# Performance work log

Hardware: AMD Instinct MI355X
Metric: run time of the kernel (lower is better)

Reference implementation:

```python
import jax, jax.numpy as jnp
import numpy as np

B, S, D = 2, 2048, 2048
H, KV = 16, 4
HD = D // H          # 128
QPK = H // KV        # queries per kv head


def setup_inputs() -> dict:
    key = jax.random.key(0)
    ks = jax.random.split(key, 8)
    x = jax.random.normal(ks[0], (B, S, D), jnp.float32)
    mask = jnp.zeros((1, 1, S, S), jnp.float32)  # unused (causal flash path)
    # RoPE tables: theta=10000, shape (S, HD//2)
    inv_freq = 1.0 / (10000.0 ** (jnp.arange(0, HD, 2, dtype=jnp.float32) / HD))
    freqs = jnp.outer(jnp.arange(S, dtype=jnp.float32), inv_freq)
    freqs_cos, freqs_sin = jnp.cos(freqs), jnp.sin(freqs)
    sc = 0.02
    Wq = jax.random.normal(ks[1], (D, H * HD), jnp.float32) * sc
    bq = jnp.zeros((H * HD,), jnp.float32)
    Wk = jax.random.normal(ks[2], (D, KV * HD), jnp.float32) * sc
    bk = jnp.zeros((KV * HD,), jnp.float32)
    Wv = jax.random.normal(ks[3], (D, KV * HD), jnp.float32) * sc
    bv = jnp.zeros((KV * HD,), jnp.float32)
    Wo = jax.random.normal(ks[4], (D, D), jnp.float32) * sc  # bias=False
    return dict(x=x, mask=mask, freqs_cos=freqs_cos, freqs_sin=freqs_sin,
                Wq=Wq, bq=bq, Wk=Wk, bk=bk, Wv=Wv, bv=bv, Wo=Wo)


def _rope(t, cos, sin):
    # t: [B, S, nH, HD]; interleaved-pair rotation as in apply_rope
    tr = t.reshape(t.shape[:-1] + (-1, 2))
    r, i = tr[..., 0], tr[..., 1]
    c = cos[None, :, None, :]
    s = sin[None, :, None, :]
    out = jnp.stack([r * c - i * s, r * s + i * c], axis=-1)
    return out.reshape(t.shape)


def reference(x, mask, freqs_cos, freqs_sin, Wq, bq, Wk, bk, Wv, bv, Wo):
    b, s, d = x.shape
    q = (x @ Wq + bq).reshape(b, s, H, HD)
    k = (x @ Wk + bk).reshape(b, s, KV, HD)
    v = (x @ Wv + bv).reshape(b, s, KV, HD)
    cos, sin = freqs_cos[:s], freqs_sin[:s]
    q = _rope(q, cos, sin)
    k = _rope(k, cos, sin)
    # GQA: repeat_interleave kv heads to match query heads
    k = jnp.repeat(k, QPK, axis=2)
    v = jnp.repeat(v, QPK, axis=2)
    q = q.transpose(0, 2, 1, 3)  # [B, H, S, HD]
    k = k.transpose(0, 2, 1, 3)
    v = v.transpose(0, 2, 1, 3)
    scores = jnp.einsum('bhqd,bhkd->bhqk', q, k) / jnp.sqrt(jnp.float32(HD))
    causal = jnp.tril(jnp.ones((s, s), bool))
    scores = jnp.where(causal[None, None], scores, jnp.finfo(scores.dtype).min)
    attn = jax.nn.softmax(scores, axis=-1)
    out = jnp.einsum('bhqk,bhkd->bhqd', attn, v)
    out = out.transpose(0, 2, 1, 3).reshape(b, s, d)
    return out @ Wo
```

## Files before the change

kernel.cpp:

```cpp
#include <hip/hip_runtime.h>


#define B_  2
#define S_  2048
#define D_  2048
#define H_  16
#define KV_ 4
#define HD_ 128
#define NQKV 3072

typedef unsigned short ushort_t;
typedef __attribute__((ext_vector_type(8))) __bf16 bf16x8;
typedef __attribute__((ext_vector_type(4))) float  f32x4;

__device__ __forceinline__ ushort_t f2bf(float f) {
    unsigned u = __float_as_uint(f);
    u += 0x7FFFu + ((u >> 16) & 1u);
    return (ushort_t)(u >> 16);
}
__device__ __forceinline__ float bf2f(ushort_t h) {
    return __uint_as_float(((unsigned)h) << 16);
}

__device__ __forceinline__ void g2l16(const void* g, void* l) {
    __builtin_amdgcn_global_load_lds(
        (const __attribute__((address_space(1))) unsigned int*)g,
        (__attribute__((address_space(3))) unsigned int*)l, 16, 0, 0);
}


__global__ __launch_bounds__(256) void k_cvt_x(const float* __restrict__ x,
                                               ushort_t* __restrict__ xb, int n4) {
    int i = blockIdx.x * 256 + threadIdx.x;
    if (i < n4) {
        float4 v = ((const float4*)x)[i];
        ushort4 o;
        o.x = f2bf(v.x); o.y = f2bf(v.y); o.z = f2bf(v.z); o.w = f2bf(v.w);
        ((ushort4*)xb)[i] = o;
    }
}

__global__ __launch_bounds__(256) void k_transpose(const float* __restrict__ src,
                                                   ushort_t* __restrict__ dst,
                                                   int R, int C) {
    __shared__ float tile[32][33];
    int c0 = blockIdx.x * 32, r0 = blockIdx.y * 32;
    int tx = threadIdx.x, ty = threadIdx.y;
    for (int i = ty; i < 32; i += 8)
        tile[i][tx] = src[(size_t)(r0 + i) * C + c0 + tx];
    __syncthreads();
    for (int i = ty; i < 32; i += 8)
        dst[(size_t)(c0 + i) * R + r0 + tx] = f2bf(tile[tx][i]);
}

__global__ __launch_bounds__(256) void k_bias(const float* bq, const float* bk,
                                              const float* bv, float* bb) {
    int i = blockIdx.x * 256 + threadIdx.x;
    if (i < 3072)
        bb[i] = (i < 2048) ? bq[i] : (i < 2560) ? bk[i - 2048] : bv[i - 2560];
}


__global__ __launch_bounds__(256, 3) void k_gemm(const ushort_t* __restrict__ A,
                                                 const ushort_t* __restrict__ Bt,
                                                 void* __restrict__ Cp,
                                                 const float* __restrict__ bias,
                                                 int M, int N, int K, int out_bf16) {
    __shared__ __align__(16) ushort_t As[128 * 32];
    __shared__ __align__(16) ushort_t Bs[128 * 32];
    int t = threadIdx.x;
    int w = t >> 6, lane = t & 63, quad = lane >> 4, l16 = lane & 15;
    int m0 = blockIdx.y * 128, n0 = blockIdx.x * 128;
    int wm = (w >> 1) * 64, wn = (w & 1) * 64;
    f32x4 acc[4][4] = {};

    int ldrow = t >> 2, ldcol = (t & 3) * 8;
    const ushort_t* Ag = A + (size_t)(m0 + ldrow) * K + ldcol;
    const ushort_t* Bg = Bt + (size_t)(n0 + ldrow) * K + ldcol;
    char* AsW = (char*)As + (t >> 6) * 1024;
    char* BsW = (char*)Bs + (t >> 6) * 1024;

    for (int k0 = 0; k0 < K; k0 += 32) {
        __syncthreads();
#pragma unroll
        for (int p = 0; p < 2; p++) {
            g2l16(Ag + (size_t)(p * 64) * K + k0, AsW + p * 4096);
            g2l16(Bg + (size_t)(p * 64) * K + k0, BsW + p * 4096);
        }
        __syncthreads();
        bf16x8 af[4], bfr[4];
#pragma unroll
        for (int i = 0; i < 4; i++)
            af[i] = *(const bf16x8*)(As + (wm + i * 16 + l16) * 32 + quad * 8);
#pragma unroll
        for (int j = 0; j < 4; j++)
            bfr[j] = *(const bf16x8*)(Bs + (wn + j * 16 + l16) * 32 + quad * 8);
#pragma unroll
        for (int i = 0; i < 4; i++)
#pragma unroll
            for (int j = 0; j < 4; j++)
                acc[i][j] = __builtin_amdgcn_mfma_f32_16x16x32_bf16(af[i], bfr[j], acc[i][j], 0, 0, 0);
    }
#pragma unroll
    for (int i = 0; i < 4; i++) {
        int r = m0 + wm + i * 16 + quad * 4;
#pragma unroll
        for (int j = 0; j < 4; j++) {
            int c = n0 + wn + j * 16 + l16;
            float bv_ = bias ? bias[c] : 0.f;
#pragma unroll
            for (int jr = 0; jr < 4; jr++) {
                float v = acc[i][j][jr] + bv_;
                if (out_bf16) ((ushort_t*)Cp)[(size_t)(r + jr) * N + c] = f2bf(v);
                else          ((float*)Cp)[(size_t)(r + jr) * N + c] = v;
            }
        }
    }
}


__global__ __launch_bounds__(256) void k_rope(ushort_t* __restrict__ QKV,
                                              const float* __restrict__ fc,
                                              const float* __restrict__ fs) {
    int idx = blockIdx.x * 256 + threadIdx.x;
    int row = idx / 1280;
    int c2 = idx - row * 1280;
    int s = row & (S_ - 1);
    int col = (c2 < 1024) ? (c2 * 2) : (2048 + (c2 - 1024) * 2);
    int dp = c2 & 63;
    float c = fc[s * 64 + dp], sn = fs[s * 64 + dp];
    size_t base = (size_t)row * NQKV + col;
    float r = bf2f(QKV[base]), im = bf2f(QKV[base + 1]);
    QKV[base]     = f2bf(r * c - im * sn);
    QKV[base + 1] = f2bf(r * sn + im * c);
}


__global__ __launch_bounds__(256) void k_vtrans(const ushort_t* __restrict__ QKV,
                                                ushort_t* __restrict__ Vt) {
    __shared__ ushort_t tile[32][33];
    int s0 = blockIdx.x * 32, d0 = blockIdx.y * 32, bz = blockIdx.z;
    int b = bz >> 2, kv = bz & 3;
    int tx = threadIdx.x, ty = threadIdx.y;
    for (int i = ty; i < 32; i += 8)
        tile[i][tx] = QKV[(size_t)(b * S_ + s0 + i) * NQKV + 2560 + kv * HD_ + d0 + tx];
    __syncthreads();
    for (int i = ty; i < 32; i += 8)
        Vt[((size_t)((b * KV_ + kv) * HD_ + d0 + i)) * S_ + s0 + tx] = tile[tx][i];
}


__global__ __launch_bounds__(512, 4) void k_flash(const ushort_t* __restrict__ QKV,
                                                  const ushort_t* __restrict__ Vt,
                                                  ushort_t* __restrict__ AO) {
    __shared__ __align__(16) ushort_t Ks[4 * 64 * 32];
    __shared__ __align__(16) ushort_t Vs[2 * 128 * 32];
    __shared__ __align__(16) ushort_t Ps[8 * 16 * 72];
    int h = blockIdx.y, b = blockIdx.z;
    int qt = b ? ((int)gridDim.x - 1 - (int)blockIdx.x) : (int)blockIdx.x;
    int kvh = h >> 2;
    int t = threadIdx.x, w = t >> 6, lane = t & 63, quad = lane >> 4, l16 = lane & 15;
    int qrow0 = qt * 128 + w * 16;
    const float SOFT = 0.08838834764831845f * 1.4426950408889634f;

    bf16x8 aq[4];
    {
        const ushort_t* qb = QKV + (size_t)(b * S_ + qrow0 + l16) * NQKV + h * HD_ + quad * 8;
#pragma unroll
        for (int kc = 0; kc < 4; kc++) aq[kc] = *(const bf16x8*)(qb + kc * 32);
    }
    bf16x8 vone;
#pragma unroll
    for (int i = 0; i < 8; i++) vone[i] = (__bf16)1.0f;

    f32x4 o[8] = {};
    f32x4 ol = {};
    ushort_t* Psw = Ps + w * 16 * 72;
    int gsw = (l16 >> 1) & 3;

    const ushort_t* kgb = QKV + (size_t)(b * S_) * NQKV + 2048 + kvh * HD_;
    const ushort_t* vgb = Vt + ((size_t)(b * KV_ + kvh) * HD_) * S_;

    int ktmax = 2 * qt + 1;
    for (int kt = 0; kt <= ktmax; kt++) {
        __syncthreads();
        if (t < 256) {
            int r = t >> 2, gs = (t & 3) ^ ((r >> 1) & 3);
            const ushort_t* kg = kgb + (size_t)(kt * 64 + r) * NQKV + gs * 8;
            char* KsW = (char*)Ks + (t >> 6) * 1024;
#pragma unroll
            for (int p = 0; p < 4; p++)
                g2l16(kg + p * 32, KsW + p * 4096);
        } else {
            int u = t - 256;
            int r = u >> 2, gs = (u & 3) ^ ((r >> 1) & 3);
            const ushort_t* vg = vgb + kt * 64 + gs * 8 + (size_t)r * S_;
            char* VsW = (char*)Vs + (u >> 6) * 1024;
#pragma unroll
            for (int p = 0; p < 4; p++)
                g2l16(vg + (size_t)((p & 1) * 64) * S_ + (p >> 1) * 32, VsW + p * 4096);
        }
        __syncthreads();

        if (kt * 64 > qrow0 + 15) continue;

        f32x4 sacc[4] = {};
#pragma unroll
        for (int kc = 0; kc < 4; kc++)
#pragma unroll
            for (int nb = 0; nb < 4; nb++) {
                bf16x8 bk = *(const bf16x8*)(Ks + kc * 2048 + (nb * 16 + l16) * 32 + ((quad ^ gsw) * 8));
                sacc[nb] = __builtin_amdgcn_mfma_f32_16x16x32_bf16(aq[kc], bk, sacc[nb], 0, 0, 0);
            }
        if (kt * 64 + 63 > qrow0) {
#pragma unroll
            for (int nb = 0; nb < 4; nb++)
#pragma unroll
                for (int jr = 0; jr < 4; jr++) {
                    int kcol = kt * 64 + nb * 16 + l16;
                    int qr = qrow0 + quad * 4 + jr;
                    if (kcol > qr) sacc[nb][jr] = -1e30f;
                }
        }
#pragma unroll
        for (int nb = 0; nb < 4; nb++)
#pragma unroll
            for (int jr = 0; jr < 4; jr++)
                Psw[(quad * 4 + jr) * 72 + nb * 16 + l16] = f2bf(exp2f(sacc[nb][jr] * SOFT));

        asm volatile("s_waitcnt lgkmcnt(0)" ::: "memory");

#pragma unroll
        for (int kc2 = 0; kc2 < 2; kc2++) {
            bf16x8 ap = *(const bf16x8*)(Psw + l16 * 72 + kc2 * 32 + quad * 8);
            ol = __builtin_amdgcn_mfma_f32_16x16x32_bf16(ap, vone, ol, 0, 0, 0);
#pragma unroll
            for (int db = 0; db < 8; db++) {
                bf16x8 bv = *(const bf16x8*)(Vs + kc2 * 4096 + (db * 16 + l16) * 32 + ((quad ^ gsw) * 8));
                o[db] = __builtin_amdgcn_mfma_f32_16x16x32_bf16(ap, bv, o[db], 0, 0, 0);
            }
        }
    }
#pragma unroll
    for (int jr = 0; jr < 4; jr++) {
        float inv = 1.0f / ol[jr];
        size_t rbase = (size_t)(b * S_ + qrow0 + quad * 4 + jr) * D_ + h * HD_;
#pragma unroll
        for (int db = 0; db < 8; db++)
            AO[rbase + db * 16 + l16] = f2bf(o[db][jr] * inv);
    }
}


extern "C" void kernel_launch(void* const* d_in, const int* in_sizes, int n_in,
                              void* d_out, int out_size, void* d_ws, size_t ws_size,
                              hipStream_t stream) {
    const float* x  = (const float*)d_in[0];
    const float* fc = (const float*)d_in[2];
    const float* fs = (const float*)d_in[3];
    const float* Wq = (const float*)d_in[4];
    const float* bq = (const float*)d_in[5];
    const float* Wk = (const float*)d_in[6];
    const float* bk = (const float*)d_in[7];
    const float* Wv = (const float*)d_in[8];
    const float* bv = (const float*)d_in[9];
    const float* Wo = (const float*)d_in[10];

    char* ws = (char*)d_ws;
    ushort_t* xb  = (ushort_t*)(ws);
    ushort_t* Wt  = (ushort_t*)(ws + 16777216);
    ushort_t* Wot = (ushort_t*)(ws + 29360128);
    float*    bb  = (float*)   (ws + 37748736);
    ushort_t* QKV = (ushort_t*)(ws + 37761024);
    ushort_t* Vt  = Wt;
    ushort_t* AO  = xb;
    float* out = (float*)d_out;

    dim3 tb(32, 8);
    k_cvt_x<<<8192, 256, 0, stream>>>(x, xb, 2097152);
    k_transpose<<<dim3(64, 64), tb, 0, stream>>>(Wq, Wt, 2048, 2048);
    k_transpose<<<dim3(16, 64), tb, 0, stream>>>(Wk, Wt + (size_t)2048 * 2048, 2048, 512);
    k_transpose<<<dim3(16, 64), tb, 0, stream>>>(Wv, Wt + (size_t)2560 * 2048, 2048, 512);
    k_transpose<<<dim3(64, 64), tb, 0, stream>>>(Wo, Wot, 2048, 2048);
    k_bias<<<12, 256, 0, stream>>>(bq, bk, bv, bb);

    k_gemm<<<dim3(24, 32), 256, 0, stream>>>(xb, Wt, QKV, bb, 4096, 3072, 2048, 1);
    k_rope<<<20480, 256, 0, stream>>>(QKV, fc, fs);
    k_vtrans<<<dim3(64, 4, 8), tb, 0, stream>>>(QKV, Vt);
    k_flash<<<dim3(16, 16, 2), 512, 0, stream>>>(QKV, Vt, AO);
    k_gemm<<<dim3(16, 32), 256, 0, stream>>>(AO, Wot, out, nullptr, 4096, 2048, 2048, 0);
}
```

Baseline: 353.3 us.

## Fuse prep kernels, fold RoPE into QKV GEMM epilogue, double-buffer flash K/V

Merges the x conversion, four weight transposes and the bias concat into one launch. RoPE moves into the QKV GEMM epilogue, pairing even and odd columns with a lane shuffle, so the separate read-modify-write pass over QKV goes away. The flash kernel now double-buffers its K/V shared-memory tiles so the next tile's global-to-LDS loads overlap compute, with one barrier per iteration. The cost is twice the K/V LDS, which may reduce occupancy, and the P buffer pitch drops from 72 to 64, which may add bank conflicts.

```diff
diff --git a/kernel.cpp b/kernel.cpp
--- a/kernel.cpp
+++ b/kernel.cpp
@@ -29,23 +29,38 @@
 }
 
 
-__global__ __launch_bounds__(256) void k_cvt_x(const float* __restrict__ x,
-                                               ushort_t* __restrict__ xb, int n4) {
-    int i = blockIdx.x * 256 + threadIdx.x;
-    if (i < n4) {
+__global__ __launch_bounds__(256) void k_prep(
+    const float* __restrict__ x,  ushort_t* __restrict__ xb,
+    const float* __restrict__ Wq, const float* __restrict__ Wk,
+    const float* __restrict__ Wv, const float* __restrict__ Wo,
+    ushort_t* __restrict__ Wt, ushort_t* __restrict__ Wot,
+    const float* __restrict__ bq, const float* __restrict__ bk,
+    const float* __restrict__ bv, float* __restrict__ bb) {
+    __shared__ float tile[32][33];
+    int id = blockIdx.x, t = threadIdx.x;
+    if (id < 8192) {
+        int i = id * 256 + t;
         float4 v = ((const float4*)x)[i];
         ushort4 o;
         o.x = f2bf(v.x); o.y = f2bf(v.y); o.z = f2bf(v.z); o.w = f2bf(v.w);
         ((ushort4*)xb)[i] = o;
-    }
-}
-
-__global__ __launch_bounds__(256) void k_transpose(const float* __restrict__ src,
-                                                   ushort_t* __restrict__ dst,
-                                                   int R, int C) {
-    __shared__ float tile[32][33];
-    int c0 = blockIdx.x * 32, r0 = blockIdx.y * 32;
-    int tx = threadIdx.x, ty = threadIdx.y;
+        return;
+    }
+    const float* src; ushort_t* dst; int C, bid;
+    if (id < 12288)      { src = Wq; dst = Wt;                       C = 2048; bid = id - 8192;  }
+    else if (id < 13312) { src = Wk; dst = Wt + (size_t)2048 * 2048; C = 512;  bid = id - 12288; }
+    else if (id < 14336) { src = Wv; dst = Wt + (size_t)2560 * 2048; C = 512;  bid = id - 13312; }
+    else if (id < 18432) { src = Wo; dst = Wot;                      C = 2048; bid = id - 14336; }
+    else {
+        int i = (id - 18432) * 256 + t;
+        if (i < 3072)
+            bb[i] = (i < 2048) ? bq[i] : (i < 2560) ? bk[i - 2048] : bv[i - 2560];
+        return;
+    }
+    const int R = 2048;
+    int nbc = C >> 5;
+    int c0 = (bid % nbc) * 32, r0 = (bid / nbc) * 32;
+    int tx = t & 31, ty = t >> 5;
     for (int i = ty; i < 32; i += 8)
         tile[i][tx] = src[(size_t)(r0 + i) * C + c0 + tx];
     __syncthreads();
@@ -53,18 +68,13 @@
         dst[(size_t)(c0 + i) * R + r0 + tx] = f2bf(tile[tx][i]);
 }
 
-__global__ __launch_bounds__(256) void k_bias(const float* bq, const float* bk,
-                                              const float* bv, float* bb) {
-    int i = blockIdx.x * 256 + threadIdx.x;
-    if (i < 3072)
-        bb[i] = (i < 2048) ? bq[i] : (i < 2560) ? bk[i - 2048] : bv[i - 2560];
-}
-
 
 __global__ __launch_bounds__(256, 3) void k_gemm(const ushort_t* __restrict__ A,
                                                  const ushort_t* __restrict__ Bt,
                                                  void* __restrict__ Cp,
                                                  const float* __restrict__ bias,
+                                                 const float* __restrict__ fc,
+                                                 const float* __restrict__ fs,
                                                  int M, int N, int K, int out_bf16) {
     __shared__ __align__(16) ushort_t As[128 * 32];
     __shared__ __align__(16) ushort_t Bs[128 * 32];
@@ -111,28 +121,18 @@
 #pragma unroll
             for (int jr = 0; jr < 4; jr++) {
                 float v = acc[i][j][jr] + bv_;
+                if (fc && c < 2560) {
+                    int s  = (r + jr) & (S_ - 1);
+                    int dp = (c & 127) >> 1;
+                    float cs = fc[s * 64 + dp], sn = fs[s * 64 + dp];
+                    float p = __shfl_xor(v, 1);
+                    v = (c & 1) ? (v * cs + p * sn) : (v * cs - p * sn);
+                }
                 if (out_bf16) ((ushort_t*)Cp)[(size_t)(r + jr) * N + c] = f2bf(v);
                 else          ((float*)Cp)[(size_t)(r + jr) * N + c] = v;
             }
         }
     }
-}
-
-
-__global__ __launch_bounds__(256) void k_rope(ushort_t* __restrict__ QKV,
-                                              const float* __restrict__ fc,
-                                              const float* __restrict__ fs) {
-    int idx = blockIdx.x * 256 + threadIdx.x;
-    int row = idx / 1280;
-    int c2 = idx - row * 1280;
-    int s = row & (S_ - 1);
-    int col = (c2 < 1024) ? (c2 * 2) : (2048 + (c2 - 1024) * 2);
-    int dp = c2 & 63;
-    float c = fc[s * 64 + dp], sn = fs[s * 64 + dp];
-    size_t base = (size_t)row * NQKV + col;
-    float r = bf2f(QKV[base]), im = bf2f(QKV[base + 1]);
-    QKV[base]     = f2bf(r * c - im * sn);
-    QKV[base + 1] = f2bf(r * sn + im * c);
 }
 
 
@@ -153,9 +153,9 @@
 __global__ __launch_bounds__(512, 4) void k_flash(const ushort_t* __restrict__ QKV,
                                                   const ushort_t* __restrict__ Vt,
                                                   ushort_t* __restrict__ AO) {
-    __shared__ __align__(16) ushort_t Ks[4 * 64 * 32];
-    __shared__ __align__(16) ushort_t Vs[2 * 128 * 32];
-    __shared__ __align__(16) ushort_t Ps[8 * 16 * 72];
+    __shared__ __align__(16) ushort_t Ks[2 * 8192];
+    __shared__ __align__(16) ushort_t Vs[2 * 8192];
+    __shared__ __align__(16) ushort_t Ps[8 * 16 * 64];
     int h = blockIdx.y, b = blockIdx.z;
     int qt = b ? ((int)gridDim.x - 1 - (int)blockIdx.x) : (int)blockIdx.x;
     int kvh = h >> 2;
@@ -175,72 +175,92 @@
 
     f32x4 o[8] = {};
     f32x4 ol = {};
-    ushort_t* Psw = Ps + w * 16 * 72;
+    ushort_t* Psw = Ps + w * 16 * 64;
     int gsw = (l16 >> 1) & 3;
 
     const ushort_t* kgb = QKV + (size_t)(b * S_) * NQKV + 2048 + kvh * HD_;
     const ushort_t* vgb = Vt + ((size_t)(b * KV_ + kvh) * HD_) * S_;
 
+    int sr, sgs; char *sK0, *sV0;
+    if (t < 256) {
+        sr = t >> 2; sgs = (t & 3) ^ ((sr >> 1) & 3);
+        sK0 = (char*)Ks + (t >> 6) * 1024;
+        sV0 = nullptr;
+    } else {
+        int u = t - 256;
+        sr = u >> 2; sgs = (u & 3) ^ ((sr >> 1) & 3);
+        sV0 = (char*)Vs + ((t - 256) >> 6) * 1024;
+        sK0 = nullptr;
+    }
+
+#define STAGE(KT, BUF)                                                          \
+    do {                                                                        \
+        if (t < 256) {                                                          \
+            const ushort_t* kg = kgb + (size_t)((KT) * 64 + sr) * NQKV + sgs * 8; \
+            char* KsW = sK0 + (BUF) * 16384;                                    \
+            _Pragma("unroll")                                                   \
+            for (int p = 0; p < 4; p++) g2l16(kg + p * 32, KsW + p * 4096);     \
+        } else {                                                                \
+            const ushort_t* vg = vgb + (KT) * 64 + sgs * 8 + (size_t)sr * S_;   \
+            char* VsW = sV0 + (BUF) * 16384;                                    \
+            _Pragma("unroll")                                                   \
+            for (int p = 0; p < 4; p++)                                         \
+                g2l16(vg + (size_t)((p & 1) * 64) * S_ + (p >> 1) * 32, VsW + p * 4096); \
+        }                                                                       \
+    } while (0)
+
     int ktmax = 2 * qt + 1;
+    STAGE(0, 0);
+    __syncthreads();
+
     for (int kt = 0; kt <= ktmax; kt++) {
-        __syncthreads();
-        if (t < 256) {
-            int r = t >> 2, gs = (t & 3) ^ ((r >> 1) & 3);
-            const ushort_t* kg = kgb + (size_t)(kt * 64 + r) * NQKV + gs * 8;
-            char* KsW = (char*)Ks + (t >> 6) * 1024;
-#pragma unroll
-            for (int p = 0; p < 4; p++)
-                g2l16(kg + p * 32, KsW + p * 4096);
-        } else {
-            int u = t - 256;
-            int r = u >> 2, gs = (u & 3) ^ ((r >> 1) & 3);
-            const ushort_t* vg = vgb + kt * 64 + gs * 8 + (size_t)r * S_;
-            char* VsW = (char*)Vs + (u >> 6) * 1024;
-#pragma unroll
-            for (int p = 0; p < 4; p++)
-                g2l16(vg + (size_t)((p & 1) * 64) * S_ + (p >> 1) * 32, VsW + p * 4096);
+        int cur = kt & 1;
+        if (kt < ktmax) STAGE(kt + 1, cur ^ 1);
+
+        if (kt * 64 <= qrow0 + 15) {
+            const ushort_t* Kc = Ks + cur * 8192;
+            const ushort_t* Vc = Vs + cur * 8192;
+            f32x4 sacc[4] = {};
+#pragma unroll
+            for (int kc = 0; kc < 4; kc++)
+#pragma unroll
+                for (int nb = 0; nb < 4; nb++) {
+                    bf16x8 bk = *(const bf16x8*)(Kc + kc * 2048 + (nb * 16 + l16) * 32 + ((quad ^ gsw) * 8));
+                    sacc[nb] = __builtin_amdgcn_mfma_f32_16x16x32_bf16(aq[kc], bk, sacc[nb], 0, 0, 0);
+                }
+            if (kt * 64 + 63 > qrow0) {
+#pragma unroll
+                for (int nb = 0; nb < 4; nb++)
+#pragma unroll
+                    for (int jr = 0; jr < 4; jr++) {
+                        int kcol = kt * 64 + nb * 16 + l16;
+                        int qr = qrow0 + quad * 4 + jr;
+                        if (kcol > qr) sacc[nb][jr] = -1e30f;
+                    }
+            }
+#pragma unroll
+            for (int nb = 0; nb < 4; nb++)
+#pragma unroll
+                for (int jr = 0; jr < 4; jr++)
+                    Psw[(quad * 4 + jr) * 64 + nb * 16 + l16] = f2bf(exp2f(sacc[nb][jr] * SOFT));
+
+            asm volatile("s_waitcnt lgkmcnt(0)" ::: "memory");
+
+#pragma unroll
+            for (int kc2 = 0; kc2 < 2; kc2++) {
+                bf16x8 ap = *(const bf16x8*)(Psw + l16 * 64 + kc2 * 32 + quad * 8);
+                ol = __builtin_amdgcn_mfma_f32_16x16x32_bf16(ap, vone, ol, 0, 0, 0);
+#pragma unroll
+                for (int db = 0; db < 8; db++) {
+                    bf16x8 bv = *(const bf16x8*)(Vc + kc2 * 4096 + (db * 16 + l16) * 32 + ((quad ^ gsw) * 8));
+                    o[db] = __builtin_amdgcn_mfma_f32_16x16x32_bf16(ap, bv, o[db], 0, 0, 0);
+                }
+            }
         }
         __syncthreads();
-
-        if (kt * 64 > qrow0 + 15) continue;
-
-        f32x4 sacc[4] = {};
-#pragma unroll
-        for (int kc = 0; kc < 4; kc++)
-#pragma unroll
-            for (int nb = 0; nb < 4; nb++) {
-                bf16x8 bk = *(const bf16x8*)(Ks + kc * 2048 + (nb * 16 + l16) * 32 + ((quad ^ gsw) * 8));
-                sacc[nb] = __builtin_amdgcn_mfma_f32_16x16x32_bf16(aq[kc], bk, sacc[nb], 0, 0, 0);
-            }
-        if (kt * 64 + 63 > qrow0) {
-#pragma unroll
-            for (int nb = 0; nb < 4; nb++)
-#pragma unroll
-                for (int jr = 0; jr < 4; jr++) {
-                    int kcol = kt * 64 + nb * 16 + l16;
-                    int qr = qrow0 + quad * 4 + jr;
-                    if (kcol > qr) sacc[nb][jr] = -1e30f;
-                }
-        }
-#pragma unroll
-        for (int nb = 0; nb < 4; nb++)
-#pragma unroll
-            for (int jr = 0; jr < 4; jr++)
-                Psw[(quad * 4 + jr) * 72 + nb * 16 + l16] = f2bf(exp2f(sacc[nb][jr] * SOFT));
-
-        asm volatile("s_waitcnt lgkmcnt(0)" ::: "memory");
-
-#pragma unroll
-        for (int kc2 = 0; kc2 < 2; kc2++) {
-            bf16x8 ap = *(const bf16x8*)(Psw + l16 * 72 + kc2 * 32 + quad * 8);
-            ol = __builtin_amdgcn_mfma_f32_16x16x32_bf16(ap, vone, ol, 0, 0, 0);
-#pragma unroll
-            for (int db = 0; db < 8; db++) {
-                bf16x8 bv = *(const bf16x8*)(Vs + kc2 * 4096 + (db * 16 + l16) * 32 + ((quad ^ gsw) * 8));
-                o[db] = __builtin_amdgcn_mfma_f32_16x16x32_bf16(ap, bv, o[db], 0, 0, 0);
-            }
-        }
-    }
+    }
+#undef STAGE
+
 #pragma unroll
     for (int jr = 0; jr < 4; jr++) {
         float inv = 1.0f / ol[jr];
@@ -276,17 +296,10 @@
     ushort_t* AO  = xb;
     float* out = (float*)d_out;
 
-    dim3 tb(32, 8);
-    k_cvt_x<<<8192, 256, 0, stream>>>(x, xb, 2097152);
-    k_transpose<<<dim3(64, 64), tb, 0, stream>>>(Wq, Wt, 2048, 2048);
-    k_transpose<<<dim3(16, 64), tb, 0, stream>>>(Wk, Wt + (size_t)2048 * 2048, 2048, 512);
-    k_transpose<<<dim3(16, 64), tb, 0, stream>>>(Wv, Wt + (size_t)2560 * 2048, 2048, 512);
-    k_transpose<<<dim3(64, 64), tb, 0, stream>>>(Wo, Wot, 2048, 2048);
-    k_bias<<<12, 256, 0, stream>>>(bq, bk, bv, bb);
-
-    k_gemm<<<dim3(24, 32), 256, 0, stream>>>(xb, Wt, QKV, bb, 4096, 3072, 2048, 1);
-    k_rope<<<20480, 256, 0, stream>>>(QKV, fc, fs);
-    k_vtrans<<<dim3(64, 4, 8), tb, 0, stream>>>(QKV, Vt);
+    k_prep<<<18444, 256, 0, stream>>>(x, xb, Wq, Wk, Wv, Wo, Wt, Wot, bq, bk, bv, bb);
+    k_gemm<<<dim3(24, 32), 256, 0, stream>>>(xb, Wt, QKV, bb, fc, fs, 4096, 3072, 2048, 1);
+    k_vtrans<<<dim3(64, 4, 8), dim3(32, 8), 0, stream>>>(QKV, Vt);
     k_flash<<<dim3(16, 16, 2), 512, 0, stream>>>(QKV, Vt, AO);
-    k_gemm<<<dim3(16, 32), 256, 0, stream>>>(AO, Wot, out, nullptr, 4096, 2048, 2048, 0);
-}
+    k_gemm<<<dim3(16, 32), 256, 0, stream>>>(AO, Wot, out, nullptr, nullptr, nullptr,
+                                             4096, 2048, 2048, 0);
+}
```

After: 340.2 us. 1.04x faster.
